# Performance work log

Hardware: AMD Instinct MI355X
Metric: run time of the kernel (lower is better)

## Reference

```python
import jax, jax.numpy as jnp
import numpy as np


def _lstm_cell(x, h, c, W_ih, W_hh, b_ih, b_hh):
    # PyTorch LSTM cell, gate order (i, f, g, o)
    gates = x @ W_ih.T + b_ih + h @ W_hh.T + b_hh
    i, f, g, o = jnp.split(gates, 4, axis=-1)
    c = jax.nn.sigmoid(f) * c + jax.nn.sigmoid(i) * jnp.tanh(g)
    h = jax.nn.sigmoid(o) * jnp.tanh(c)
    return h, c


def setup_inputs() -> dict:
    key = jax.random.key(0)
    B, T, F, H = 512, 256, 128, 512
    ks = jax.random.split(key, 12)
    s = 1.0 / np.sqrt(H)  # PyTorch-style uniform-ish scale (use scaled normal)
    inp = {
        'ts_batch': jax.random.normal(ks[0], (B, T, F), jnp.float32),
        'enc_W_ih': jax.random.normal(ks[1], (4 * H, F), jnp.float32) * s,
        'enc_W_hh': jax.random.normal(ks[2], (4 * H, H), jnp.float32) * s,
        'enc_b_ih': jax.random.normal(ks[3], (4 * H,), jnp.float32) * s,
        'enc_b_hh': jax.random.normal(ks[4], (4 * H,), jnp.float32) * s,
        'dec_W_ih': jax.random.normal(ks[5], (4 * H, F), jnp.float32) * s,
        'dec_W_hh': jax.random.normal(ks[6], (4 * H, H), jnp.float32) * s,
        'dec_b_ih': jax.random.normal(ks[7], (4 * H,), jnp.float32) * s,
        'dec_b_hh': jax.random.normal(ks[8], (4 * H,), jnp.float32) * s,
        'Wo': jax.random.normal(ks[9], (F, H), jnp.float32) * s,
        'bo': jax.random.normal(ks[10], (F,), jnp.float32) * s,
    }
    return inp


def reference(ts_batch, enc_W_ih, enc_W_hh, enc_b_ih, enc_b_hh,
              dec_W_ih, dec_W_hh, dec_b_ih, dec_b_hh, Wo, bo):
    B, T, F = ts_batch.shape
    H = enc_W_hh.shape[1]
    dt = ts_batch.dtype
    h0 = jnp.zeros((B, H), dt)
    c0 = jnp.zeros((B, H), dt)

    # --- encoder: standard LSTM over time, keep final hidden state ---
    def enc_step(carry, x_t):
        h, c = carry
        h, c = _lstm_cell(x_t, h, c, enc_W_ih, enc_W_hh, enc_b_ih, enc_b_hh)
        return (h, c), None

    xs = jnp.swapaxes(ts_batch, 0, 1)  # [T, B, F]
    (h_enc, _), _ = jax.lax.scan(enc_step, (h0, c0), xs)

    # --- decoder: free-running (eval mode), iterating i = T-1 .. 0 ---
    # at each step: emit y = Linear(h), then feed y through decoder LSTM
    def dec_step(carry, _):
        h, c = carry
        y = h @ Wo.T + bo  # [B, F]
        h, c = _lstm_cell(y, h, c, dec_W_ih, dec_W_hh, dec_b_ih, dec_b_hh)
        return (h, c), y

    _, ys = jax.lax.scan(dec_step, (h_enc, c0), None, length=T)  # [T, B, F]
    # ys[0] corresponds to output[:, T-1], ys[T-1] to output[:, 0] -> flip
    output = jnp.flip(jnp.swapaxes(ys, 0, 1), axis=1)  # [B, T, F]
    return output
```

## Files before the change

### kernel.cpp

```cpp
#include <hip/hip_runtime.h>

#define Bn 512
#define Tn 256
#define Fn 128
#define Hn 512
#define KIE 20
#define KID 16
#define NWG 256
#define RS 648

typedef __attribute__((ext_vector_type(8))) __bf16 bf16x8;
typedef __attribute__((ext_vector_type(4))) float floatx4;
typedef __attribute__((ext_vector_type(4))) unsigned uintx4;

__device__ __forceinline__ unsigned short f2bf_u16(float f) {
  union { float f; unsigned u; } v; v.f = f;
  unsigned r = v.u + 0x7FFFu + ((v.u >> 16) & 1u);
  return (unsigned short)(r >> 16);
}

__device__ __forceinline__ float sigm(float x) {
  return __builtin_amdgcn_rcpf(1.f + __expf(-x));
}
__device__ __forceinline__ float ftanh(float x) {
  return 1.f - 2.f * __builtin_amdgcn_rcpf(1.f + __expf(2.f * x));
}

__global__ void pack_enc_k(const float* __restrict__ Wih, const float* __restrict__ Whh,
                           unsigned short* __restrict__ Bpe) {
  int id = blockIdx.x;
  int nt = id / KIE, ki = id % KIE;
  int l = threadIdx.x;
  int n = nt * 16 + (l & 15);
  int kb = ki * 32 + (l >> 4) * 8;
  __align__(16) unsigned short o[8];
#pragma unroll
  for (int j = 0; j < 8; ++j) {
    int k = kb + j;
    float v = (k < Fn) ? Wih[n * Fn + k] : Whh[n * Hn + (k - Fn)];
    o[j] = f2bf_u16(v);
  }
  *(uint4*)(Bpe + (size_t)(id * 64 + l) * 8) = *(uint4*)o;
}

__global__ void pack_dec_k(const float* __restrict__ Wih, const float* __restrict__ Whh,
                           const float* __restrict__ Wo, unsigned short* __restrict__ Bpd) {
  int id = blockIdx.x;
  int nt = id / KID, ki = id % KID;
  int l = threadIdx.x;
  int n = nt * 16 + (l & 15);
  int kb = ki * 32 + (l >> 4) * 8;
  float acc[8];
#pragma unroll
  for (int j = 0; j < 8; ++j) acc[j] = Whh[n * Hn + kb + j];
  for (int f = 0; f < Fn; ++f) {
    float wf = Wih[n * Fn + f];
    const float* wo = Wo + f * Hn + kb;
#pragma unroll
    for (int j = 0; j < 8; ++j) acc[j] += wf * wo[j];
  }
  __align__(16) unsigned short o[8];
#pragma unroll
  for (int j = 0; j < 8; ++j) o[j] = f2bf_u16(acc[j]);
  *(uint4*)(Bpd + (size_t)(id * 64 + l) * 8) = *(uint4*)o;
}

__global__ void pack_wo_k(const float* __restrict__ Wo, unsigned short* __restrict__ Bpw) {
  int id = blockIdx.x;
  int ft = id / KID, ki = id % KID;
  int l = threadIdx.x;
  int f = ft * 16 + (l & 15);
  int kb = ki * 32 + (l >> 4) * 8;
  __align__(16) unsigned short o[8];
#pragma unroll
  for (int j = 0; j < 8; ++j) o[j] = f2bf_u16(Wo[f * Hn + kb + j]);
  *(uint4*)(Bpw + (size_t)(id * 64 + l) * 8) = *(uint4*)o;
}

__global__ void bias_k(const float* __restrict__ ebih, const float* __restrict__ ebhh,
                       const float* __restrict__ dbih, const float* __restrict__ dbhh,
                       const float* __restrict__ dWih, const float* __restrict__ bo,
                       float* __restrict__ benc, float* __restrict__ bdec) {
  int n = blockIdx.x * blockDim.x + threadIdx.x;
  benc[n] = ebih[n] + ebhh[n];
  float a = dbih[n] + dbhh[n];
  for (int f = 0; f < Fn; ++f) a += dWih[n * Fn + f] * bo[f];
  bdec[n] = a;
}

__global__ void pack_x_k(const float* __restrict__ ts, unsigned short* __restrict__ xp) {
  size_t i = (size_t)blockIdx.x * 256 + threadIdx.x;
  int k4 = (int)(i & 31);
  size_t bs = i >> 5;
  int s = (int)(bs & 255);
  size_t b = bs >> 8;
  float4 v = *(const float4*)(ts + (i << 2));
  __align__(8) unsigned short o[4];
  o[0] = f2bf_u16(v.x); o[1] = f2bf_u16(v.y); o[2] = f2bf_u16(v.z); o[3] = f2bf_u16(v.w);
  *(unsigned long long*)(xp + ((size_t)s * Bn + b) * Fn + k4 * 4) = *(unsigned long long*)o;
}

__global__ void init_k(unsigned long long* __restrict__ Hg0,
                       unsigned* __restrict__ flgA, unsigned* __restrict__ flgB,
                       unsigned* __restrict__ xcdP) {
  int i = blockIdx.x * 256 + threadIdx.x;
  Hg0[i] = 0ULL;
  if (i < 8192) { flgA[i] = 0u; flgB[i] = 0u; }
  if (i < NWG) xcdP[i] = 0xFFu;
}

#define POLL(F, p) do { \
  if (l < 16) { \
    const unsigned* fp_ = (F) + (size_t)(mg * 16 + l) * 32; \
    while (__hip_atomic_load(fp_, __ATOMIC_RELAXED, __HIP_MEMORY_SCOPE_AGENT) < (unsigned)(p)) \
      __builtin_amdgcn_s_sleep(1); \
  } \
  __asm__ __volatile__("" ::: "memory"); \
} while (0)

#define SETF(F, p) do { if (tid == 0) \
  __hip_atomic_store((F) + (size_t)gid * 32, (unsigned)(p), __ATOMIC_RELAXED, __HIP_MEMORY_SCOPE_AGENT); \
} while (0)

#define STAGE_H2(OFF, curbuf) do { \
  const unsigned short* sp_ = Hg + (size_t)(curbuf) * (Bn * Hn) + (size_t)(b0 + sh_r) * Hn + sh_c * 32; \
  uintx4 t0_, t1_, t2_, t3_; \
  if (loc) { \
    asm volatile("global_load_dwordx4 %0, %4, off sc0\n\t" \
                 "global_load_dwordx4 %1, %4, off offset:16 sc0\n\t" \
                 "global_load_dwordx4 %2, %4, off offset:32 sc0\n\t" \
                 "global_load_dwordx4 %3, %4, off offset:48 sc0\n\t" \
                 "s_waitcnt vmcnt(0)" \
                 : "=&v"(t0_), "=&v"(t1_), "=&v"(t2_), "=&v"(t3_) : "v"(sp_) : "memory"); \
  } else { \
    const unsigned long long* src_ = (const unsigned long long*)sp_; \
    unsigned long long v_[8]; \
    _Pragma("unroll") for (int u_ = 0; u_ < 8; ++u_) \
      v_[u_] = __hip_atomic_load(src_ + u_, __ATOMIC_RELAXED, __HIP_MEMORY_SCOPE_AGENT); \
    t0_[0] = (unsigned)v_[0]; t0_[1] = (unsigned)(v_[0] >> 32); t0_[2] = (unsigned)v_[1]; t0_[3] = (unsigned)(v_[1] >> 32); \
    t1_[0] = (unsigned)v_[2]; t1_[1] = (unsigned)(v_[2] >> 32); t1_[2] = (unsigned)v_[3]; t1_[3] = (unsigned)(v_[3] >> 32); \
    t2_[0] = (unsigned)v_[4]; t2_[1] = (unsigned)(v_[4] >> 32); t2_[2] = (unsigned)v_[5]; t2_[3] = (unsigned)(v_[5] >> 32); \
    t3_[0] = (unsigned)v_[6]; t3_[1] = (unsigned)(v_[6] >> 32); t3_[2] = (unsigned)v_[7]; t3_[3] = (unsigned)(v_[7] >> 32); \
  } \
  uintx4* dst_ = (uintx4*)&A_lds[sh_r * RS + (OFF) + sh_c * 32]; \
  dst_[0] = t0_; dst_[1] = t1_; dst_[2] = t2_; dst_[3] = t3_; \
} while (0)

#define STAGE_X2(s_) do { \
  uint4 xv_ = *(const uint4*)(xp + ((size_t)(s_) * Bn + b0 + sh_r) * Fn + sh_c * 8); \
  *(uint4*)&A_lds[sh_r * RS + sh_c * 8] = xv_; \
} while (0)

#define MFMA_GATES2(BR, KN) do { \
  floatx4 a0_ = {0.f, 0.f, 0.f, 0.f}, a1_ = {0.f, 0.f, 0.f, 0.f}; \
  const unsigned short* Ar0_ = &A_lds[l15 * RS + q * 8]; \
  const unsigned short* Ar1_ = &A_lds[(l15 + 16) * RS + q * 8]; \
  _Pragma("unroll") for (int k = 0; k < (KN); ++k) { \
    bf16x8 b_ = (BR)[k]; \
    a0_ = __builtin_amdgcn_mfma_f32_16x16x32_bf16(*(const bf16x8*)(Ar0_ + k * 32), b_, a0_, 0, 0, 0); \
    a1_ = __builtin_amdgcn_mfma_f32_16x16x32_bf16(*(const bf16x8*)(Ar1_ + k * 32), b_, a1_, 0, 0, 0); \
  } \
  _Pragma("unroll") for (int r = 0; r < 4; ++r) { \
    gates_lds[g_][q * 4 + r][nsub * 16 + l15] = a0_[r]; \
    gates_lds[g_][16 + q * 4 + r][nsub * 16 + l15] = a1_[r]; \
  } \
} while (0)

#define MFMA_GATES2_Y(BR, sd) do { \
  floatx4 a0_ = {0.f, 0.f, 0.f, 0.f}, a1_ = {0.f, 0.f, 0.f, 0.f}; \
  floatx4 ay_ = {0.f, 0.f, 0.f, 0.f}; \
  const unsigned short* Ar0_ = &A_lds[l15 * RS + q * 8]; \
  const unsigned short* Ar1_ = &A_lds[(l15 + 16) * RS + q * 8]; \
  const unsigned short* Ay_ = yA ? Ar0_ : Ar1_; \
  _Pragma("unroll") for (int k = 0; k < KID; ++k) { \
    bf16x8 b_ = (BR)[k]; \
    a0_ = __builtin_amdgcn_mfma_f32_16x16x32_bf16(*(const bf16x8*)(Ar0_ + k * 32), b_, a0_, 0, 0, 0); \
    a1_ = __builtin_amdgcn_mfma_f32_16x16x32_bf16(*(const bf16x8*)(Ar1_ + k * 32), b_, a1_, 0, 0, 0); \
    if (doY) ay_ = __builtin_amdgcn_mfma_f32_16x16x32_bf16( \
        *(const bf16x8*)(Ay_ + k * 32), *(const bf16x8*)&Bw_lds[(k * 64 + l) * 8], ay_, 0, 0, 0); \
  } \
  _Pragma("unroll") for (int r = 0; r < 4; ++r) { \
    gates_lds[g_][q * 4 + r][nsub * 16 + l15] = a0_[r]; \
    gates_lds[g_][16 + q * 4 + r][nsub * 16 + l15] = a1_[r]; \
  } \
  if (doY) { \
    _Pragma("unroll") for (int r = 0; r < 4; ++r) \
      __builtin_nontemporal_store(ay_[r] + bof, \
        out + ((size_t)(ybase + q * 4 + r) * Tn + (Tn - 1 - (sd))) * Fn + ns * 16 + l15); \
  } \
} while (0)

#define EPI2(BI, BF, BG, BO, nxtbuf) do { \
  float gi0_ = gates_lds[0][eb][ej] + (BI); \
  float gf0_ = gates_lds[1][eb][ej] + (BF); \
  float gg0_ = gates_lds[2][eb][ej] + (BG); \
  float go0_ = gates_lds[3][eb][ej] + (BO); \
  cA = sigm(gf0_) * cA + sigm(gi0_) * ftanh(gg0_); \
  float h0_ = sigm(go0_) * ftanh(cA); \
  float gi1_ = gates_lds[0][eb + 16][ej] + (BI); \
  float gf1_ = gates_lds[1][eb + 16][ej] + (BF); \
  float gg1_ = gates_lds[2][eb + 16][ej] + (BG); \
  float go1_ = gates_lds[3][eb + 16][ej] + (BO); \
  cB = sigm(gf1_) * cB + sigm(gi1_) * ftanh(gg1_); \
  float h1_ = sigm(go1_) * ftanh(cB); \
  unsigned short hv0_ = f2bf_u16(h0_), hv1_ = f2bf_u16(h1_); \
  unsigned short* hp0_ = Hg + (size_t)(nxtbuf) * (Bn * Hn) + (size_t)(b0 + eb) * Hn + j0 + ej; \
  unsigned short* hp1_ = hp0_ + 16 * Hn; \
  if (loc) { *hp0_ = hv0_; *hp1_ = hv1_; } \
  else { \
    __hip_atomic_store(hp0_, hv0_, __ATOMIC_RELAXED, __HIP_MEMORY_SCOPE_AGENT); \
    __hip_atomic_store(hp1_, hv1_, __ATOMIC_RELAXED, __HIP_MEMORY_SCOPE_AGENT); \
  } \
} while (0)

__global__ __launch_bounds__(512, 2) void lstm_persist(
    const unsigned short* __restrict__ xp,
    const unsigned short* __restrict__ Bpe,
    const unsigned short* __restrict__ Bpd,
    const unsigned short* __restrict__ Bpw,
    const float* __restrict__ benc,
    const float* __restrict__ bdec,
    const float* __restrict__ bo,
    unsigned short* __restrict__ Hg,
    unsigned* __restrict__ flgA,
    unsigned* __restrict__ flgB,
    unsigned* __restrict__ xcdPub,
    float* __restrict__ out)
{
  const int wg = blockIdx.x;
  const int tid = threadIdx.x;
  const int w = tid >> 6, l = tid & 63;
  const int l15 = l & 15, q = l >> 4;
  const int g_ = w >> 1, nsub = w & 1;
  const int eb = tid >> 5, ej = tid & 31;
  const int sh_r = tid >> 4, sh_c = tid & 15;

  const int grp = wg & 7, rank = wg >> 3;
  const int mg = grp * 2 + (rank >> 4);
  const int ns = rank & 15;
  const int gid = mg * 16 + ns;
  const int b0 = mg * 32, j0 = ns * 32;
  const int nt = g_ * 32 + ns * 2 + nsub;

  __shared__ __align__(16) unsigned short A_lds[32 * RS];
  __shared__ __align__(16) float gates_lds[4][32][34];
  __shared__ __align__(16) unsigned short Bw_lds[KID * 64 * 8];
  __shared__ int sh_asn[2];

  if (tid == 0) {
    unsigned x_;
    asm volatile("s_getreg_b32 %0, hwreg(HW_REG_XCC_ID)" : "=s"(x_));
    x_ &= 15u;
    sh_asn[1] = (int)x_;
    __hip_atomic_store(&xcdPub[wg], x_, __ATOMIC_RELAXED, __HIP_MEMORY_SCOPE_AGENT);
  }
  __syncthreads();
  const unsigned myx = (unsigned)sh_asn[1];
  if (tid < 64) {
    int ok = 1;
    if (tid < 16) {
      const int phys = grp + 8 * ((mg & 1) * 16 + tid);
      unsigned v_ = 0xFFu;
      for (int it = 0; it < 32768; ++it) {
        v_ = __hip_atomic_load(&xcdPub[phys], __ATOMIC_RELAXED, __HIP_MEMORY_SCOPE_AGENT);
        if (v_ != 0xFFu) break;
        __builtin_amdgcn_s_sleep(2);
      }
      ok = (v_ == myx) ? 1 : 0;
    }
    int all_ = __all(ok) ? 1 : 0;
    if (tid == 0) sh_asn[0] = all_;
  }
  __syncthreads();
  const int loc = sh_asn[0];

  bf16x8 Bq[KIE], Bd[KID];
  {
    const bf16x8* p = (const bf16x8*)Bpe + (size_t)nt * (KIE * 64) + l;
#pragma unroll
    for (int k = 0; k < KIE; ++k) Bq[k] = p[k * 64];
  }
  {
    const bf16x8* p = (const bf16x8*)Bpd + (size_t)nt * (KID * 64) + l;
#pragma unroll
    for (int k = 0; k < KID; ++k) Bd[k] = p[k * 64];
  }
  const float bie = benc[0 * Hn + j0 + ej], bfe = benc[1 * Hn + j0 + ej];
  const float bge = benc[2 * Hn + j0 + ej], boe = benc[3 * Hn + j0 + ej];
  const float bid = bdec[0 * Hn + j0 + ej], bfd = bdec[1 * Hn + j0 + ej];
  const float bgd = bdec[2 * Hn + j0 + ej], bod = bdec[3 * Hn + j0 + ej];

  if (ns < 8) {
    const uint4* src = (const uint4*)(Bpw + (size_t)ns * (KID * 64 * 8));
    uint4* dst = (uint4*)Bw_lds;
    dst[tid * 2] = src[tid * 2];
    dst[tid * 2 + 1] = src[tid * 2 + 1];
  }
  const bool yA = (ns < 8) && (w == 0);
  const bool yB = (ns < 8) && (w == 4);
  const bool doY = yA || yB;
  const int ybase = yA ? b0 : b0 + 16;
  float bof = 0.f;
  if (doY) bof = bo[ns * 16 + l15];

  float cA = 0.f, cB = 0.f;

  __syncthreads();

  for (int s = 0; s < Tn; ++s) {
    const int cur = s & 1, nxt = cur ^ 1;
    POLL(flgA, s);
    STAGE_X2(s);
    STAGE_H2(Fn, cur);
    __syncthreads();
    MFMA_GATES2(Bq, KIE);
    __syncthreads();
    EPI2(bie, bfe, bge, boe, nxt);
    __syncthreads();
    SETF(flgA, s + 1);
  }

  cA = 0.f; cB = 0.f;
  for (int sd = 0; sd < Tn; ++sd) {
    const int phg = Tn + sd;
    const int cur = phg & 1, nxt = cur ^ 1;
    POLL(flgA, phg);
    STAGE_H2(0, cur);
    __syncthreads();
    MFMA_GATES2_Y(Bd, sd);
    __syncthreads();
    EPI2(bid, bfd, bgd, bod, nxt);
    __syncthreads();
    SETF(flgA, phg + 1);
  }
}

extern "C" void kernel_launch(void* const* d_in, const int* in_sizes, int n_in,
                              void* d_out, int out_size, void* d_ws, size_t ws_size,
                              hipStream_t stream) {
  const float* ts   = (const float*)d_in[0];
  const float* eWih = (const float*)d_in[1];
  const float* eWhh = (const float*)d_in[2];
  const float* ebih = (const float*)d_in[3];
  const float* ebhh = (const float*)d_in[4];
  const float* dWih = (const float*)d_in[5];
  const float* dWhh = (const float*)d_in[6];
  const float* dbih = (const float*)d_in[7];
  const float* dbhh = (const float*)d_in[8];
  const float* Wo   = (const float*)d_in[9];
  const float* bo   = (const float*)d_in[10];
  float* outp = (float*)d_out;

  char* ws = (char*)d_ws;
  unsigned short* Bpe  = (unsigned short*)(ws);
  unsigned short* Bpd  = (unsigned short*)(ws + 2621440);
  unsigned short* Bpw  = (unsigned short*)(ws + 4718592);
  float*          benc = (float*)(ws + 4849664);
  float*          bdec = (float*)(ws + 4857856);
  unsigned short* Hg   = (unsigned short*)(ws + 4866048);
  unsigned*       flgA = (unsigned*)(ws + 5914624);
  unsigned*       flgB = (unsigned*)(ws + 5947392);
  unsigned short* xp   = (unsigned short*)(ws + 5980160);
  unsigned*       xcdP = (unsigned*)outp;

  pack_enc_k<<<128 * KIE, 64, 0, stream>>>(eWih, eWhh, Bpe);
  pack_dec_k<<<128 * KID, 64, 0, stream>>>(dWih, dWhh, Wo, Bpd);
  pack_wo_k<<<8 * KID, 64, 0, stream>>>(Wo, Bpw);
  bias_k<<<8, 256, 0, stream>>>(ebih, ebhh, dbih, dbhh, dWih, bo, benc, bdec);
  pack_x_k<<<16384, 256, 0, stream>>>(ts, xp);
  init_k<<<256, 256, 0, stream>>>((unsigned long long*)Hg, flgA, flgB, xcdP);

  lstm_persist<<<NWG, 512, 0, stream>>>(xp, Bpe, Bpd, Bpw, benc, bdec, bo, Hg,
                                        flgA, flgB, xcdP, outp);
}
```

Before: 1.926 ms.

## Switch gate GEMM to 32x32x16 MFMA with split-K across wave halves

Replaces the pair of 16x16x32 MFMA accumulators per wave with a single 32x32x16 bf16 MFMA tile per gate. The K dimension is split between two groups of four waves, and partial sums are combined through LDS atomic adds into gates_lds, which the epilogue zeroes after reading. Weight packing is changed to the 32-wide N layout, and the decoder's output projection now runs on the gate-3 waves after their gate MFMAs. The aim is fewer MFMA instructions and better MFMA throughput per step, at the cost of LDS atomic contention and extra zeroing stores on the serial recurrent path.

```diff
diff --git a/kernel.cpp b/kernel.cpp
--- a/kernel.cpp
+++ b/kernel.cpp
@@ -4,13 +4,17 @@
 #define Tn 256
 #define Fn 128
 #define Hn 512
-#define KIE 20
+#define KIE32 40
+#define KID32 32
+#define EH 20
+#define DH 16
 #define KID 16
 #define NWG 256
 #define RS 648
 
 typedef __attribute__((ext_vector_type(8))) __bf16 bf16x8;
 typedef __attribute__((ext_vector_type(4))) float floatx4;
+typedef __attribute__((ext_vector_type(16))) float floatx16;
 typedef __attribute__((ext_vector_type(4))) unsigned uintx4;
 
 __device__ __forceinline__ unsigned short f2bf_u16(float f) {
@@ -29,10 +33,10 @@
 __global__ void pack_enc_k(const float* __restrict__ Wih, const float* __restrict__ Whh,
                            unsigned short* __restrict__ Bpe) {
   int id = blockIdx.x;
-  int nt = id / KIE, ki = id % KIE;
+  int nt = id / KIE32, ki = id % KIE32;
   int l = threadIdx.x;
-  int n = nt * 16 + (l & 15);
-  int kb = ki * 32 + (l >> 4) * 8;
+  int n = nt * 32 + (l & 31);
+  int kb = ki * 16 + (l >> 5) * 8;
   __align__(16) unsigned short o[8];
 #pragma unroll
   for (int j = 0; j < 8; ++j) {
@@ -46,10 +50,10 @@
 __global__ void pack_dec_k(const float* __restrict__ Wih, const float* __restrict__ Whh,
                            const float* __restrict__ Wo, unsigned short* __restrict__ Bpd) {
   int id = blockIdx.x;
-  int nt = id / KID, ki = id % KID;
+  int nt = id / KID32, ki = id % KID32;
   int l = threadIdx.x;
-  int n = nt * 16 + (l & 15);
-  int kb = ki * 32 + (l >> 4) * 8;
+  int n = nt * 32 + (l & 31);
+  int kb = ki * 16 + (l >> 5) * 8;
   float acc[8];
 #pragma unroll
   for (int j = 0; j < 8; ++j) acc[j] = Whh[n * Hn + kb + j];
@@ -151,43 +155,26 @@
   *(uint4*)&A_lds[sh_r * RS + sh_c * 8] = xv_; \
 } while (0)
 
-#define MFMA_GATES2(BR, KN) do { \
-  floatx4 a0_ = {0.f, 0.f, 0.f, 0.f}, a1_ = {0.f, 0.f, 0.f, 0.f}; \
-  const unsigned short* Ar0_ = &A_lds[l15 * RS + q * 8]; \
-  const unsigned short* Ar1_ = &A_lds[(l15 + 16) * RS + q * 8]; \
-  _Pragma("unroll") for (int k = 0; k < (KN); ++k) { \
-    bf16x8 b_ = (BR)[k]; \
-    a0_ = __builtin_amdgcn_mfma_f32_16x16x32_bf16(*(const bf16x8*)(Ar0_ + k * 32), b_, a0_, 0, 0, 0); \
-    a1_ = __builtin_amdgcn_mfma_f32_16x16x32_bf16(*(const bf16x8*)(Ar1_ + k * 32), b_, a1_, 0, 0, 0); \
+#define MFMA_G32(BR, KN) do { \
+  floatx16 a_ = {0.f}; \
+  const unsigned short* Ar_ = &A_lds[l31 * RS + (kh * (KN)) * 16 + ksub]; \
+  _Pragma("unroll") for (int t = 0; t < (KN); ++t) \
+    a_ = __builtin_amdgcn_mfma_f32_32x32x16_bf16(*(const bf16x8*)(Ar_ + t * 16), (BR)[t], a_, 0, 0, 0); \
+  _Pragma("unroll") for (int r = 0; r < 16; ++r) { \
+    int row_ = (r & 3) + 8 * (r >> 2) + 4 * lhi; \
+    __hip_atomic_fetch_add(&gates_lds[g2][row_][l31], a_[r], __ATOMIC_RELAXED, __HIP_MEMORY_SCOPE_WORKGROUP); \
   } \
-  _Pragma("unroll") for (int r = 0; r < 4; ++r) { \
-    gates_lds[g_][q * 4 + r][nsub * 16 + l15] = a0_[r]; \
-    gates_lds[g_][16 + q * 4 + r][nsub * 16 + l15] = a1_[r]; \
-  } \
-} while (0)
-
-#define MFMA_GATES2_Y(BR, sd) do { \
-  floatx4 a0_ = {0.f, 0.f, 0.f, 0.f}, a1_ = {0.f, 0.f, 0.f, 0.f}; \
+} while (0)
+
+#define MFMA_Y(sd) do { \
   floatx4 ay_ = {0.f, 0.f, 0.f, 0.f}; \
-  const unsigned short* Ar0_ = &A_lds[l15 * RS + q * 8]; \
-  const unsigned short* Ar1_ = &A_lds[(l15 + 16) * RS + q * 8]; \
-  const unsigned short* Ay_ = yA ? Ar0_ : Ar1_; \
-  _Pragma("unroll") for (int k = 0; k < KID; ++k) { \
-    bf16x8 b_ = (BR)[k]; \
-    a0_ = __builtin_amdgcn_mfma_f32_16x16x32_bf16(*(const bf16x8*)(Ar0_ + k * 32), b_, a0_, 0, 0, 0); \
-    a1_ = __builtin_amdgcn_mfma_f32_16x16x32_bf16(*(const bf16x8*)(Ar1_ + k * 32), b_, a1_, 0, 0, 0); \
-    if (doY) ay_ = __builtin_amdgcn_mfma_f32_16x16x32_bf16( \
+  const unsigned short* Ay_ = &A_lds[(l15 + yro) * RS + q * 8]; \
+  _Pragma("unroll") for (int k = 0; k < KID; ++k) \
+    ay_ = __builtin_amdgcn_mfma_f32_16x16x32_bf16( \
         *(const bf16x8*)(Ay_ + k * 32), *(const bf16x8*)&Bw_lds[(k * 64 + l) * 8], ay_, 0, 0, 0); \
-  } \
-  _Pragma("unroll") for (int r = 0; r < 4; ++r) { \
-    gates_lds[g_][q * 4 + r][nsub * 16 + l15] = a0_[r]; \
-    gates_lds[g_][16 + q * 4 + r][nsub * 16 + l15] = a1_[r]; \
-  } \
-  if (doY) { \
-    _Pragma("unroll") for (int r = 0; r < 4; ++r) \
-      __builtin_nontemporal_store(ay_[r] + bof, \
-        out + ((size_t)(ybase + q * 4 + r) * Tn + (Tn - 1 - (sd))) * Fn + ns * 16 + l15); \
-  } \
+  _Pragma("unroll") for (int r = 0; r < 4; ++r) \
+    __builtin_nontemporal_store(ay_[r] + bof, \
+      out + ((size_t)(b0 + yro + q * 4 + r) * Tn + (Tn - 1 - (sd))) * Fn + ns * 16 + l15); \
 } while (0)
 
 #define EPI2(BI, BF, BG, BO, nxtbuf) do { \
@@ -195,12 +182,16 @@
   float gf0_ = gates_lds[1][eb][ej] + (BF); \
   float gg0_ = gates_lds[2][eb][ej] + (BG); \
   float go0_ = gates_lds[3][eb][ej] + (BO); \
-  cA = sigm(gf0_) * cA + sigm(gi0_) * ftanh(gg0_); \
-  float h0_ = sigm(go0_) * ftanh(cA); \
   float gi1_ = gates_lds[0][eb + 16][ej] + (BI); \
   float gf1_ = gates_lds[1][eb + 16][ej] + (BF); \
   float gg1_ = gates_lds[2][eb + 16][ej] + (BG); \
   float go1_ = gates_lds[3][eb + 16][ej] + (BO); \
+  gates_lds[0][eb][ej] = 0.f; gates_lds[1][eb][ej] = 0.f; \
+  gates_lds[2][eb][ej] = 0.f; gates_lds[3][eb][ej] = 0.f; \
+  gates_lds[0][eb + 16][ej] = 0.f; gates_lds[1][eb + 16][ej] = 0.f; \
+  gates_lds[2][eb + 16][ej] = 0.f; gates_lds[3][eb + 16][ej] = 0.f; \
+  cA = sigm(gf0_) * cA + sigm(gi0_) * ftanh(gg0_); \
+  float h0_ = sigm(go0_) * ftanh(cA); \
   cB = sigm(gf1_) * cB + sigm(gi1_) * ftanh(gg1_); \
   float h1_ = sigm(go1_) * ftanh(cB); \
   unsigned short hv0_ = f2bf_u16(h0_), hv1_ = f2bf_u16(h1_); \
@@ -231,7 +222,9 @@
   const int tid = threadIdx.x;
   const int w = tid >> 6, l = tid & 63;
   const int l15 = l & 15, q = l >> 4;
-  const int g_ = w >> 1, nsub = w & 1;
+  const int l31 = l & 31, lhi = l >> 5;
+  const int g2 = w & 3, kh = w >> 2;
+  const int ksub = lhi * 8;
   const int eb = tid >> 5, ej = tid & 31;
   const int sh_r = tid >> 4, sh_c = tid & 15;
 
@@ -240,10 +233,9 @@
   const int ns = rank & 15;
   const int gid = mg * 16 + ns;
   const int b0 = mg * 32, j0 = ns * 32;
-  const int nt = g_ * 32 + ns * 2 + nsub;
 
   __shared__ __align__(16) unsigned short A_lds[32 * RS];
-  __shared__ __align__(16) float gates_lds[4][32][34];
+  __shared__ __align__(16) float gates_lds[4][32][33];
   __shared__ __align__(16) unsigned short Bw_lds[KID * 64 * 8];
   __shared__ int sh_asn[2];
 
@@ -274,16 +266,17 @@
   __syncthreads();
   const int loc = sh_asn[0];
 
-  bf16x8 Bq[KIE], Bd[KID];
+  bf16x8 Bq[EH], Bd[DH];
+  const int nt32 = g2 * 16 + ns;
   {
-    const bf16x8* p = (const bf16x8*)Bpe + (size_t)nt * (KIE * 64) + l;
-#pragma unroll
-    for (int k = 0; k < KIE; ++k) Bq[k] = p[k * 64];
+    const bf16x8* p = (const bf16x8*)Bpe + ((size_t)nt32 * KIE32 + kh * EH) * 64 + l;
+#pragma unroll
+    for (int k = 0; k < EH; ++k) Bq[k] = p[k * 64];
   }
   {
-    const bf16x8* p = (const bf16x8*)Bpd + (size_t)nt * (KID * 64) + l;
-#pragma unroll
-    for (int k = 0; k < KID; ++k) Bd[k] = p[k * 64];
+    const bf16x8* p = (const bf16x8*)Bpd + ((size_t)nt32 * KID32 + kh * DH) * 64 + l;
+#pragma unroll
+    for (int k = 0; k < DH; ++k) Bd[k] = p[k * 64];
   }
   const float bie = benc[0 * Hn + j0 + ej], bfe = benc[1 * Hn + j0 + ej];
   const float bge = benc[2 * Hn + j0 + ej], boe = benc[3 * Hn + j0 + ej];
@@ -296,12 +289,12 @@
     dst[tid * 2] = src[tid * 2];
     dst[tid * 2 + 1] = src[tid * 2 + 1];
   }
-  const bool yA = (ns < 8) && (w == 0);
-  const bool yB = (ns < 8) && (w == 4);
-  const bool doY = yA || yB;
-  const int ybase = yA ? b0 : b0 + 16;
+  const bool doY = (ns < 8) && (g2 == 3);
+  const int yro = kh ? 16 : 0;
   float bof = 0.f;
   if (doY) bof = bo[ns * 16 + l15];
+
+  for (int i = tid; i < 4 * 32 * 33; i += 512) ((float*)gates_lds)[i] = 0.f;
 
   float cA = 0.f, cB = 0.f;
 
@@ -313,7 +306,7 @@
     STAGE_X2(s);
     STAGE_H2(Fn, cur);
     __syncthreads();
-    MFMA_GATES2(Bq, KIE);
+    MFMA_G32(Bq, EH);
     __syncthreads();
     EPI2(bie, bfe, bge, boe, nxt);
     __syncthreads();
@@ -327,7 +320,8 @@
     POLL(flgA, phg);
     STAGE_H2(0, cur);
     __syncthreads();
-    MFMA_GATES2_Y(Bd, sd);
+    MFMA_G32(Bd, DH);
+    if (doY) MFMA_Y(sd);
     __syncthreads();
     EPI2(bid, bfd, bgd, bod, nxt);
     __syncthreads();
@@ -363,8 +357,8 @@
   unsigned short* xp   = (unsigned short*)(ws + 5980160);
   unsigned*       xcdP = (unsigned*)outp;
 
-  pack_enc_k<<<128 * KIE, 64, 0, stream>>>(eWih, eWhh, Bpe);
-  pack_dec_k<<<128 * KID, 64, 0, stream>>>(dWih, dWhh, Wo, Bpd);
+  pack_enc_k<<<64 * KIE32, 64, 0, stream>>>(eWih, eWhh, Bpe);
+  pack_dec_k<<<64 * KID32, 64, 0, stream>>>(dWih, dWhh, Wo, Bpd);
   pack_wo_k<<<8 * KID, 64, 0, stream>>>(Wo, Bpw);
   bias_k<<<8, 256, 0, stream>>>(ebih, ebhh, dbih, dbhh, dWih, bo, benc, bdec);
   pack_x_k<<<16384, 256, 0, stream>>>(ts, xp);
```

Result: slower. 6.868 ms (+256.6%).
